# Kernel optimization log

Measured on AMD Instinct MI355X. Metric: run time of the kernel, lower is better.

Reference implementation:

```python
import jax, jax.numpy as jnp
import numpy as np

HUGE = jnp.float32(1e31)  # ops.HUGE_INT


def setup_inputs() -> dict:
    key = jax.random.key(0)
    ks = jax.random.split(key, 11)
    B, A = 2048, 256
    NE, NR = 100000, 1000
    DE, DR, DH = 128, 128, 256
    act = DE + DR  # action_dim = W1 hidden width
    return {
        "e": jax.random.randint(ks[0], (B,), 0, NE),
        "q": jax.random.randint(ks[1], (B,), 0, NR),
        "H": jax.random.normal(ks[2], (B, DH), jnp.float32),
        "r_space": jax.random.randint(ks[3], (B, A), 0, NR),
        "r_mask": jnp.ones((B, A), jnp.float32),
        "entity_emb": jax.random.normal(ks[4], (NE, DE), jnp.float32),
        "rel_emb": jax.random.normal(ks[5], (NR, DR), jnp.float32),
        "W1": jax.random.normal(ks[6], (DE + DH + DR, act), jnp.float32) * 0.05,
        "b1": jnp.zeros((act,), jnp.float32),
        "W2": jax.random.normal(ks[7], (act, DR), jnp.float32) * 0.05,
        "b2": jnp.zeros((DR,), jnp.float32),
    }


def reference(e, q, H, r_space, r_mask, entity_emb, rel_emb, W1, b1, W2, b2):
    # Gather node / query embeddings (kg.get_entity_embeddings / get_relation_embeddings)
    E = entity_emb[e]              # [B, DE]
    Q = rel_emb[q]                 # [B, DR]
    X = jnp.concatenate([E, H, Q], axis=-1)        # [B, DE+DH+DR]
    X = jax.nn.relu(X @ W1 + b1)                   # W1 + ReLU
    X = X @ W2 + b2                                # W2 -> [B, DR]
    # Gather candidate relation embeddings for the (padded) action space
    R = rel_emb[r_space]                           # [B, A, DR]
    logit = jnp.einsum("bad,bd->ba", R, X)        # squeeze(R @ X.unsqueeze(2))
    logit = logit - (1.0 - r_mask) * HUGE          # mask invalid actions
    dist = jax.nn.softmax(logit, axis=-1)          # [B, A]
    entropy = -jnp.sum(dist * jnp.log(jnp.clip(dist, 1e-20, None)), axis=-1)  # ops.entropy
    return dist, entropy
```

## Files before the change

### kernel.cpp

```cpp
#include <hip/hip_runtime.h>


#define DE   128
#define DH   256
#define DR   128
#define DIN  512
#define ACT  256
#define AA   256
#define BB   8
#define NR   1000
#define SCL  1008

#define XS_P 520
#define HS_P 264
#define X2_P 136

#define W2B_OFF 16384
#define RB_OFF  20480
#define PREP_T  36608

typedef __attribute__((ext_vector_type(4))) float f32x4;
typedef __attribute__((ext_vector_type(8))) short s16x8;
typedef unsigned int u32;
typedef unsigned short u16;

#define MFMA(a,b,c) __builtin_amdgcn_mfma_f32_16x16x32_bf16(a, b, c, 0, 0, 0)

__device__ __forceinline__ u32 b16(float x) {
    u32 u = __float_as_uint(x);
    return (u + 0x7FFFu + ((u >> 16) & 1u)) >> 16;
}
__device__ __forceinline__ float b16f(u32 h) { return __uint_as_float(h << 16); }
__device__ __forceinline__ u32 pack2(float a, float b) { return b16(a) | (b16(b) << 16); }

__device__ __forceinline__ s16x8 asfrag(uint4 v) {
    union { uint4 u; s16x8 s; } c; c.u = v; return c.s;
}

__global__ __launch_bounds__(256) void prep_kernel(
    const float* __restrict__ W1, const float* __restrict__ W2,
    const float* __restrict__ rel_emb, uint4* __restrict__ wsb)
{
    const int id = blockIdx.x * 256 + threadIdx.x;
    const int l  = id & 63;
    const int tl = id >> 6;
    const int kb_l = (l >> 4) * 8;
    const int n_l  = l & 15;
    float f[8];
    if (tl < 256) {
        const int kt = tl >> 4, nt = tl & 15;
        const int kb = kt * 32 + kb_l, n = nt * 16 + n_l;
        #pragma unroll
        for (int i = 0; i < 8; ++i) f[i] = W1[(size_t)(kb + i) * ACT + n];
    } else if (tl < 320) {
        const int t2 = tl - 256;
        const int kt = t2 >> 3, nt = t2 & 7;
        const int kb = kt * 32 + kb_l, n = nt * 16 + n_l;
        #pragma unroll
        for (int i = 0; i < 8; ++i) f[i] = W2[(size_t)(kb + i) * DR + n];
    } else {
        const int t3 = tl - 320;
        const int nt = t3 >> 2, kt = t3 & 3;
        const int kb = kt * 32 + kb_l, n = nt * 16 + n_l;
        #pragma unroll
        for (int i = 0; i < 8; ++i)
            f[i] = (n < NR) ? rel_emb[(size_t)n * DR + kb + i] : 0.f;
    }
    uint4 o;
    o.x = pack2(f[0], f[1]); o.y = pack2(f[2], f[3]);
    o.z = pack2(f[4], f[5]); o.w = pack2(f[6], f[7]);
    wsb[id] = o;
}

__global__ __launch_bounds__(1024, 2) void policy_kernel(
    const int*   __restrict__ e,
    const int*   __restrict__ q,
    const float* __restrict__ H,
    const int*   __restrict__ r_space,
    const float* __restrict__ r_mask,
    const float* __restrict__ entity_emb,
    const float* __restrict__ rel_emb,
    const float* __restrict__ b1,
    const float* __restrict__ b2,
    const uint4* __restrict__ wsb,
    float* __restrict__ dist_out,
    float* __restrict__ ent_out)
{
    const int t  = threadIdx.x;
    const int b0 = blockIdx.x * BB;
    const int l  = t & 63;
    const int w  = t >> 6;
    const int m  = l & 15;
    const int pl = m >> 3;
    const int rw = m & 7;
    const int kb_l = (l >> 4) * 8;

    __shared__ __align__(16) u16 xbf[2][BB][XS_P];
    __shared__ __align__(16) u16 hbf[2][BB][HS_P];
    __shared__ __align__(16) u16 x2bf[2][BB][X2_P];
    __shared__ float scoreL[BB * SCL];

    int   ridx[4];
    float msk [4];
    if (w < 8) {
        #pragma unroll
        for (int c = 0; c < 4; ++c) {
            ridx[c] = r_space[(size_t)(b0 + w) * AA + l + 64 * c];
            msk [c] = r_mask [(size_t)(b0 + w) * AA + l + 64 * c];
        }
    }

    {
        const int row = t & 7;
        const int kq  = (t >> 3) * 4;
        const int sb  = b0 + row;
        float4 v;
        if (kq < DE)            v = *(const float4*)&entity_emb[(size_t)e[sb] * DE + kq];
        else if (kq < DE + DH)  v = *(const float4*)&H[(size_t)sb * DH + (kq - DE)];
        else                    v = *(const float4*)&rel_emb[(size_t)q[sb] * DR + (kq - DE - DH)];
        const float f[4] = {v.x, v.y, v.z, v.w};
        u32 hi[4], lo[4];
        #pragma unroll
        for (int i = 0; i < 4; ++i) {
            hi[i] = b16(f[i]);
            lo[i] = b16(f[i] - b16f(hi[i]));
        }
        uint2 ph, plv;
        ph.x  = hi[0] | (hi[1] << 16); ph.y  = hi[2] | (hi[3] << 16);
        plv.x = lo[0] | (lo[1] << 16); plv.y = lo[2] | (lo[3] << 16);
        *(uint2*)&xbf[0][row][kq] = ph;
        *(uint2*)&xbf[1][row][kq] = plv;
    }
    __syncthreads();

    {
        f32x4 acc = {0.f, 0.f, 0.f, 0.f};
        const u16* abase = &xbf[pl][rw][kb_l];
        #pragma unroll
        for (int kt = 0; kt < 16; ++kt) {
            const uint4 af = *(const uint4*)(abase + kt * 32);
            const uint4 bv = wsb[(size_t)(kt * 16 + w) * 64 + l];
            acc = MFMA(asfrag(af), asfrag(bv), acc);
        }
        #pragma unroll
        for (int v = 0; v < 4; ++v)
            acc[v] += __shfl_xor(acc[v], 32, 64);
        if (l < 32) {
            const int r4 = (l >> 4) * 4;
            const int n  = w * 16 + m;
            const float bb = b1[n];
            #pragma unroll
            for (int v = 0; v < 4; ++v) {
                const float h = fmaxf(acc[v] + bb, 0.f);
                const u32 hh = b16(h);
                hbf[0][r4 + v][n] = (u16)hh;
                hbf[1][r4 + v][n] = (u16)b16(h - b16f(hh));
            }
        }
    }
    __syncthreads();

    if (w < 8) {
        f32x4 acc = {0.f, 0.f, 0.f, 0.f};
        const u16* abase = &hbf[pl][rw][kb_l];
        #pragma unroll
        for (int kt = 0; kt < 8; ++kt) {
            const uint4 af = *(const uint4*)(abase + kt * 32);
            const uint4 bv = wsb[(size_t)(W2B_OFF + (kt * 8 + w) * 64 + l)];
            acc = MFMA(asfrag(af), asfrag(bv), acc);
        }
        #pragma unroll
        for (int v = 0; v < 4; ++v) acc[v] += __shfl_xor(acc[v], 32, 64);
        if (l < 32) {
            const int r4 = (l >> 4) * 4;
            const int n  = w * 16 + m;
            const float bb = b2[n];
            #pragma unroll
            for (int v = 0; v < 4; ++v) {
                const float x2 = acc[v] + bb;
                const u32 xh = b16(x2);
                x2bf[0][r4 + v][n] = (u16)xh;
                x2bf[1][r4 + v][n] = (u16)b16(x2 - b16f(xh));
            }
        }
    }
    __syncthreads();

    {
        uint4 sf[4];
        const u16* abase = &x2bf[pl][rw][kb_l];
        #pragma unroll
        for (int kt = 0; kt < 4; ++kt)
            sf[kt] = *(const uint4*)(abase + kt * 32);
        #pragma unroll
        for (int i = 0; i < 4; ++i) {
            const int nt = w * 4 + i;
            if (nt >= 63) break;
            f32x4 acc = {0.f, 0.f, 0.f, 0.f};
            #pragma unroll
            for (int kt = 0; kt < 4; ++kt) {
                const uint4 bv = wsb[(size_t)(RB_OFF + (nt * 4 + kt) * 64 + l)];
                acc = MFMA(asfrag(sf[kt]), asfrag(bv), acc);
            }
            #pragma unroll
            for (int v = 0; v < 4; ++v) acc[v] += __shfl_xor(acc[v], 32, 64);
            if (l < 32) {
                const int r4 = (l >> 4) * 4;
                const int n  = nt * 16 + m;
                #pragma unroll
                for (int v = 0; v < 4; ++v)
                    scoreL[(r4 + v) * SCL + n] = acc[v];
            }
        }
    }
    __syncthreads();

    if (w < 8) {
        float lg[4];
        #pragma unroll
        for (int c = 0; c < 4; ++c)
            lg[c] = scoreL[w * SCL + ridx[c]] - (1.0f - msk[c]) * 1e31f;

        float mx = fmaxf(fmaxf(lg[0], lg[1]), fmaxf(lg[2], lg[3]));
        #pragma unroll
        for (int off = 32; off >= 1; off >>= 1)
            mx = fmaxf(mx, __shfl_xor(mx, off, 64));

        float p[4], S = 0.f, SLa = 0.f;
        #pragma unroll
        for (int c = 0; c < 4; ++c) {
            const float z = lg[c] - mx;
            p[c] = __expf(z);
            S   += p[c];
            SLa += p[c] * z;
        }
        #pragma unroll
        for (int off = 32; off >= 1; off >>= 1) {
            S   += __shfl_xor(S,   off, 64);
            SLa += __shfl_xor(SLa, off, 64);
        }

        const float inv = 1.0f / S;
        #pragma unroll
        for (int c = 0; c < 4; ++c)
            dist_out[(size_t)(b0 + w) * AA + l + 64 * c] = p[c] * inv;
        if (l == 0)
            ent_out[b0 + w] = __logf(S) - SLa * inv;
    }
}

extern "C" void kernel_launch(void* const* d_in, const int* in_sizes, int n_in,
                              void* d_out, int out_size, void* d_ws, size_t ws_size,
                              hipStream_t stream) {
    const int*   e          = (const int*)  d_in[0];
    const int*   q          = (const int*)  d_in[1];
    const float* H          = (const float*)d_in[2];
    const int*   r_space    = (const int*)  d_in[3];
    const float* r_mask     = (const float*)d_in[4];
    const float* entity_emb = (const float*)d_in[5];
    const float* rel_emb    = (const float*)d_in[6];
    const float* W1         = (const float*)d_in[7];
    const float* b1         = (const float*)d_in[8];
    const float* W2         = (const float*)d_in[9];
    const float* b2         = (const float*)d_in[10];

    const int B = in_sizes[0];
    float* dist_out = (float*)d_out;
    float* ent_out  = (float*)d_out + (size_t)B * AA;
    uint4* wsb      = (uint4*)d_ws;

    prep_kernel<<<PREP_T / 256, 256, 0, stream>>>(W1, W2, rel_emb, wsb);
    policy_kernel<<<B / BB, 1024, 0, stream>>>(
        e, q, H, r_space, r_mask, entity_emb, rel_emb,
        b1, b2, wsb, dist_out, ent_out);
}
```

Measured before the change: 20.26 us.

## Prefetch weight fragments before barriers and split bf16 plane writes across lanes

Issues global loads for the first few weight fragments of each MFMA stage before the preceding __syncthreads, so their latency overlaps the barrier and the prior stage's epilogue. The epilogue writes of the hi and lo bf16 planes are spread across all 64 lanes instead of only 32. The launch-bounds occupancy hint rises from 2 to 4 blocks per CU, and the prep kernel uses 1024-thread blocks with a bounds check. The risks are higher register pressure from the prefetch buffers, and the occupancy hint may force spills or have no effect given the LDS footprint.

```diff
diff --git a/kernel.cpp b/kernel.cpp
--- a/kernel.cpp
+++ b/kernel.cpp
@@ -37,11 +37,12 @@
     union { uint4 u; s16x8 s; } c; c.u = v; return c.s;
 }
 
-__global__ __launch_bounds__(256) void prep_kernel(
+__global__ __launch_bounds__(1024) void prep_kernel(
     const float* __restrict__ W1, const float* __restrict__ W2,
     const float* __restrict__ rel_emb, uint4* __restrict__ wsb)
 {
-    const int id = blockIdx.x * 256 + threadIdx.x;
+    const int id = blockIdx.x * 1024 + threadIdx.x;
+    if (id >= PREP_T) return;
     const int l  = id & 63;
     const int tl = id >> 6;
     const int kb_l = (l >> 4) * 8;
@@ -72,7 +73,7 @@
     wsb[id] = o;
 }
 
-__global__ __launch_bounds__(1024, 2) void policy_kernel(
+__global__ __launch_bounds__(1024, 4) void policy_kernel(
     const int*   __restrict__ e,
     const int*   __restrict__ q,
     const float* __restrict__ H,
@@ -94,6 +95,8 @@
     const int pl = m >> 3;
     const int rw = m & 7;
     const int kb_l = (l >> 4) * 8;
+    const int eplane = l >> 5;
+    const int er4    = ((l >> 4) & 1) * 4;
 
     __shared__ __align__(16) u16 xbf[2][BB][XS_P];
     __shared__ __align__(16) u16 hbf[2][BB][HS_P];
@@ -131,6 +134,11 @@
         *(uint2*)&xbf[0][row][kq] = ph;
         *(uint2*)&xbf[1][row][kq] = plv;
     }
+
+    uint4 bpre1[4];
+    #pragma unroll
+    for (int kt = 0; kt < 4; ++kt)
+        bpre1[kt] = wsb[(size_t)(kt * 16 + w) * 64 + l];
     __syncthreads();
 
     {
@@ -139,24 +147,31 @@
         #pragma unroll
         for (int kt = 0; kt < 16; ++kt) {
             const uint4 af = *(const uint4*)(abase + kt * 32);
-            const uint4 bv = wsb[(size_t)(kt * 16 + w) * 64 + l];
+            const uint4 bv = (kt < 4) ? bpre1[kt]
+                                      : wsb[(size_t)(kt * 16 + w) * 64 + l];
             acc = MFMA(asfrag(af), asfrag(bv), acc);
         }
         #pragma unroll
         for (int v = 0; v < 4; ++v)
             acc[v] += __shfl_xor(acc[v], 32, 64);
-        if (l < 32) {
-            const int r4 = (l >> 4) * 4;
+        {
             const int n  = w * 16 + m;
             const float bb = b1[n];
             #pragma unroll
             for (int v = 0; v < 4; ++v) {
                 const float h = fmaxf(acc[v] + bb, 0.f);
                 const u32 hh = b16(h);
-                hbf[0][r4 + v][n] = (u16)hh;
-                hbf[1][r4 + v][n] = (u16)b16(h - b16f(hh));
-            }
-        }
+                const u16 out = eplane ? (u16)b16(h - b16f(hh)) : (u16)hh;
+                hbf[eplane][er4 + v][n] = out;
+            }
+        }
+    }
+    uint4 bpre2[2];
+    {
+        const int w2 = w & 7;
+        #pragma unroll
+        for (int kt = 0; kt < 2; ++kt)
+            bpre2[kt] = wsb[(size_t)(W2B_OFF + (kt * 8 + w2) * 64 + l)];
     }
     __syncthreads();
 
@@ -166,24 +181,28 @@
         #pragma unroll
         for (int kt = 0; kt < 8; ++kt) {
             const uint4 af = *(const uint4*)(abase + kt * 32);
-            const uint4 bv = wsb[(size_t)(W2B_OFF + (kt * 8 + w) * 64 + l)];
+            const uint4 bv = (kt < 2) ? bpre2[kt]
+                                      : wsb[(size_t)(W2B_OFF + (kt * 8 + w) * 64 + l)];
             acc = MFMA(asfrag(af), asfrag(bv), acc);
         }
         #pragma unroll
         for (int v = 0; v < 4; ++v) acc[v] += __shfl_xor(acc[v], 32, 64);
-        if (l < 32) {
-            const int r4 = (l >> 4) * 4;
+        {
             const int n  = w * 16 + m;
             const float bb = b2[n];
             #pragma unroll
             for (int v = 0; v < 4; ++v) {
                 const float x2 = acc[v] + bb;
                 const u32 xh = b16(x2);
-                x2bf[0][r4 + v][n] = (u16)xh;
-                x2bf[1][r4 + v][n] = (u16)b16(x2 - b16f(xh));
-            }
-        }
-    }
+                const u16 out = eplane ? (u16)b16(x2 - b16f(xh)) : (u16)xh;
+                x2bf[eplane][er4 + v][n] = out;
+            }
+        }
+    }
+    uint4 bpre3[4];
+    #pragma unroll
+    for (int kt = 0; kt < 4; ++kt)
+        bpre3[kt] = wsb[(size_t)(RB_OFF + ((w * 4) * 4 + kt) * 64 + l)];
     __syncthreads();
 
     {
@@ -199,7 +218,8 @@
             f32x4 acc = {0.f, 0.f, 0.f, 0.f};
             #pragma unroll
             for (int kt = 0; kt < 4; ++kt) {
-                const uint4 bv = wsb[(size_t)(RB_OFF + (nt * 4 + kt) * 64 + l)];
+                const uint4 bv = (i == 0) ? bpre3[kt]
+                                          : wsb[(size_t)(RB_OFF + (nt * 4 + kt) * 64 + l)];
                 acc = MFMA(asfrag(sf[kt]), asfrag(bv), acc);
             }
             #pragma unroll
@@ -269,7 +289,7 @@
     float* ent_out  = (float*)d_out + (size_t)B * AA;
     uint4* wsb      = (uint4*)d_ws;
 
-    prep_kernel<<<PREP_T / 256, 256, 0, stream>>>(W1, W2, rel_emb, wsb);
+    prep_kernel<<<(PREP_T + 1023) / 1024, 1024, 0, stream>>>(W1, W2, rel_emb, wsb);
     policy_kernel<<<B / BB, 1024, 0, stream>>>(
         e, q, H, r_space, r_mask, entity_emb, rel_emb,
         b1, b2, wsb, dist_out, ent_out);
```

After: 34.73 us. 71.5% more time.
